# Optimization experiments

Measured on AMD Instinct MI355X. Metric: run time of the kernel, lower is better.

The kernel has to match this reference:

```python
import jax, jax.numpy as jnp
import numpy as np

B, D, K, L, C = 1024, 512, 255, 256, 80  # batch, feat, internal nodes, leaves, classes
DEPTH = 8  # complete binary tree: 2^8 = 256 leaves


def _build_res_path():
    # res_path[l, k] = 1 if internal node k is on leaf l's path and leaf goes left,
    # -1 if it goes right, 0 if node k not on the path (matches build_tree_squeeze).
    rp = np.zeros((L, K), dtype=np.int32)
    for leaf in range(L):
        node = 0
        for d in range(DEPTH):
            bit = (leaf >> (DEPTH - 1 - d)) & 1  # 0 -> left, 1 -> right
            rp[leaf, node] = 1 if bit == 0 else -1
            node = 2 * node + 1 + bit
    return jnp.asarray(rp)


def setup_inputs() -> dict:
    key = jax.random.key(0)
    k1, k2, k3, k4 = jax.random.split(key, 4)
    x = jax.random.normal(k1, (B, D), dtype=jnp.float32)
    node_embeddings = jax.random.normal(k2, (K, D), dtype=jnp.float32)
    leaf_W = jax.random.normal(k3, (L * C, D), dtype=jnp.float32) * (1.0 / np.sqrt(D))
    leaf_b = jax.random.normal(k4, (L * C,), dtype=jnp.float32) * 0.01
    res_path = _build_res_path()
    return {"x": x, "node_embeddings": node_embeddings, "leaf_W": leaf_W,
            "leaf_b": leaf_b, "res_path": res_path}


def reference(x, node_embeddings, leaf_W, leaf_b, res_path):
    # L2-normalize node embeddings, cosine-sim routing probabilities
    ne = node_embeddings / jnp.linalg.norm(node_embeddings, axis=-1, keepdims=True)
    node_sim = jax.nn.sigmoid(jnp.einsum('bc,kc->bk', x, ne))  # [B, K]
    # leaf decision logits: Linear(D, L*C) reshaped to [B, L, C]
    leaf_dec = (jnp.einsum('bc,oc->bo', x, leaf_W) + leaf_b).reshape(x.shape[0], L, C)
    left_mask = (res_path == 1)[None]    # [1, L, K]
    right_mask = (res_path == -1)[None]  # [1, L, K]
    ns = node_sim[:, None, :]            # [B, 1, K]
    prob_left = jnp.prod(jnp.where(left_mask, ns, 1.0), axis=-1)        # [B, L]
    prob_right = jnp.prod(jnp.where(right_mask, 1.0 - ns, 1.0), axis=-1)  # [B, L]
    probs = (prob_left * prob_right)[..., None] * leaf_dec  # [B, L, C]
    return probs.sum(axis=1), node_sim
```

## Files before the change

### kernel.cpp

```cpp
#include <hip/hip_runtime.h>
#include <stdint.h>

#define B_  1024
#define D_  512
#define K_  255
#define L_  256
#define C_  80

typedef __attribute__((ext_vector_type(8))) short bf16x8;
typedef __attribute__((ext_vector_type(4))) float f32x4;
typedef __attribute__((ext_vector_type(8))) short short8;

#define GLD(gsrc, ldst) \
  __builtin_amdgcn_global_load_lds((const __attribute__((address_space(1))) void*)(gsrc), \
                                   (__attribute__((address_space(3))) void*)(ldst), 16, 0, 0)

__device__ __forceinline__ short cvt_bf16(float f) {
    unsigned u = __float_as_uint(f);
    u += 0x7FFFu + ((u >> 16) & 1u);
    return (short)(u >> 16);
}

__global__ __launch_bounds__(256) void convert_kernel(const float* __restrict__ w,
                                                      const float* __restrict__ x,
                                                      const float* __restrict__ ne,
                                                      short* __restrict__ wb,
                                                      short* __restrict__ xb,
                                                      short* __restrict__ neb) {
    __shared__ float red[256];
    const int tid = threadIdx.x;
    if (blockIdx.x < 2048) {
        size_t i0 = (size_t)blockIdx.x * 256 + tid;
        const size_t stride = 2048u * 256u;
        for (size_t v = i0; v < 1310720u; v += stride) {
            float4 a = ((const float4*)w)[v * 2];
            float4 b = ((const float4*)w)[v * 2 + 1];
            short8 o;
            o[0] = cvt_bf16(a.x); o[1] = cvt_bf16(a.y); o[2] = cvt_bf16(a.z); o[3] = cvt_bf16(a.w);
            o[4] = cvt_bf16(b.x); o[5] = cvt_bf16(b.y); o[6] = cvt_bf16(b.z); o[7] = cvt_bf16(b.w);
            ((short8*)wb)[v] = o;
        }
        for (size_t v = i0; v < 65536u; v += stride) {
            float4 a = ((const float4*)x)[v * 2];
            float4 b = ((const float4*)x)[v * 2 + 1];
            short8 o;
            o[0] = cvt_bf16(a.x); o[1] = cvt_bf16(a.y); o[2] = cvt_bf16(a.z); o[3] = cvt_bf16(a.w);
            o[4] = cvt_bf16(b.x); o[5] = cvt_bf16(b.y); o[6] = cvt_bf16(b.z); o[7] = cvt_bf16(b.w);
            ((short8*)xb)[v] = o;
        }
    } else {
        const int row = blockIdx.x - 2048;
        if (row == 255) {
            ((unsigned*)(neb + 255 * 512))[tid] = 0u;
            return;
        }
        const float2* nr = (const float2*)(ne + (size_t)row * 512);
        float2 a = nr[tid];
        red[tid] = a.x * a.x + a.y * a.y;
        __syncthreads();
        #pragma unroll
        for (int s = 128; s > 0; s >>= 1) {
            if (tid < s) red[tid] += red[tid + s];
            __syncthreads();
        }
        float inv = rsqrtf(red[0]);
        unsigned lo = (unsigned short)cvt_bf16(a.x * inv);
        unsigned hi = (unsigned short)cvt_bf16(a.y * inv);
        ((unsigned*)(neb + (size_t)row * 512))[tid] = lo | (hi << 16);
    }
}

__global__ __launch_bounds__(256) void simgemm_kernel(const short* __restrict__ xb,
                                                      const short* __restrict__ neb,
                                                      float* __restrict__ out1) {
    __shared__ __align__(16) short Ald[512 * 8];
    __shared__ __align__(16) short Bld[512 * 8];
    const int tid = threadIdx.x;
    const int lane = tid & 63, wave = tid >> 6;
    const int q = lane >> 4, r = lane & 15;
    const int mt = blockIdx.x >> 2;
    const int nt = blockIdx.x & 3;

    f32x4 acc[4];
    #pragma unroll
    for (int nf = 0; nf < 4; ++nf) acc[nf] = (f32x4){0.f, 0.f, 0.f, 0.f};

    const bf16x8* Av = (const bf16x8*)Ald;
    const bf16x8* Bv = (const bf16x8*)Bld;

    for (int kb = 0; kb < 8; ++kb) {
        __syncthreads();
        #pragma unroll
        for (int j = 0; j < 2; ++j) {
            int ph = j * 256 + tid, rr = ph >> 3, g = (ph & 7) ^ (rr & 7);
            GLD(xb + ((size_t)(mt * 64 + rr) * D_ + kb * 64 + g * 8), Ald + ph * 8);
        }
        #pragma unroll
        for (int j = 0; j < 2; ++j) {
            int ph = j * 256 + tid, cc = ph >> 3, g = (ph & 7) ^ (cc & 7);
            GLD(neb + ((size_t)(nt * 64 + cc) * D_ + kb * 64 + g * 8), Bld + ph * 8);
        }
        __syncthreads();
        #pragma unroll
        for (int ks = 0; ks < 2; ++ks) {
            const int g = ks * 4 + q;
            int rl = wave * 16 + r;
            bf16x8 af = Av[rl * 8 + (g ^ (rl & 7))];
            #pragma unroll
            for (int nf = 0; nf < 4; ++nf) {
                int cl = nf * 16 + r;
                bf16x8 bfr = Bv[cl * 8 + (g ^ (cl & 7))];
                acc[nf] = __builtin_amdgcn_mfma_f32_16x16x32_bf16(af, bfr, acc[nf], 0, 0, 0);
            }
        }
    }
    #pragma unroll
    for (int nf = 0; nf < 4; ++nf) {
        int gcol = nt * 64 + nf * 16 + r;
        if (gcol < K_) {
            #pragma unroll
            for (int i = 0; i < 4; ++i) {
                int grow = mt * 64 + wave * 16 + q * 4 + i;
                out1[(size_t)grow * K_ + gcol] = 1.f / (1.f + __expf(-acc[nf][i]));
            }
        }
    }
}

__global__ __launch_bounds__(256) void leafprob_kernel(const float* __restrict__ out1,
                                                       float* __restrict__ p_ws,
                                                       float* __restrict__ out0) {
    __shared__ float ss[K_];
    const int b = blockIdx.x, t = threadIdx.x;
    if (t < K_) ss[t] = out1[(size_t)b * K_ + t];
    if (t < C_) out0[(size_t)b * C_ + t] = 0.f;
    __syncthreads();
    float prob = 1.f;
    int node = 0;
    #pragma unroll
    for (int d = 0; d < 8; ++d) {
        int bit = (t >> (7 - d)) & 1;
        float s = ss[node];
        prob *= bit ? (1.f - s) : s;
        node = 2 * node + 1 + bit;
    }
    p_ws[(size_t)b * L_ + t] = prob;
}

__global__ __launch_bounds__(256, 2) void gemm_kernel(const short* __restrict__ xb,
                                                      const short* __restrict__ wb,
                                                      const float* __restrict__ p,
                                                      const float* __restrict__ lb,
                                                      float* __restrict__ partial) {
    __shared__ __align__(16) short Ald[2 * 1024 * 8];
    __shared__ __align__(16) short Bld[2 * 640 * 8];
    __shared__ float p_ld[128][4];

    const int tid = threadIdx.x;
    const int lane = tid & 63, wave = tid >> 6;
    const int q = lane >> 4, r = lane & 15;
    const int wrow = wave * 32;
    const int lc = blockIdx.x & 63;
    const int mt = blockIdx.x >> 6;

    if (tid < 128) {
        float4 pw = *(const float4*)(p + (size_t)(mt * 128 + tid) * L_ + lc * 4);
        p_ld[tid][0] = pw.x; p_ld[tid][1] = pw.y;
        p_ld[tid][2] = pw.z; p_ld[tid][3] = pw.w;
    }

    auto stageA = [&](int buf, int kc) {
        #pragma unroll
        for (int j = 0; j < 4; ++j) {
            int ph = j * 256 + tid;
            int rr = ph >> 3;
            int g  = (ph & 7) ^ (rr & 7);
            GLD(xb + ((size_t)(mt * 128 + rr)) * D_ + kc * 64 + g * 8,
                Ald + (buf * 1024 + ph) * 8);
        }
    };
    auto stageB = [&](int buf, int li, int kc) {
        #pragma unroll
        for (int j = 0; j < 2; ++j) {
            int ph = j * 256 + tid;
            int cc = ph >> 3;
            int g  = (ph & 7) ^ (cc & 7);
            GLD(wb + ((size_t)(lc * 4 + li) * C_ + cc) * D_ + kc * 64 + g * 8,
                Bld + (buf * 640 + ph) * 8);
        }
        if (tid < 128) {
            int ph = 512 + tid;
            int cc = ph >> 3;
            int g  = (ph & 7) ^ (cc & 7);
            GLD(wb + ((size_t)(lc * 4 + li) * C_ + cc) * D_ + kc * 64 + g * 8,
                Bld + (buf * 640 + ph) * 8);
        }
    };

    stageA(0, 0);
    stageB(0, 0, 0);
    __syncthreads();

    f32x4 outacc[2][5];
    #pragma unroll
    for (int nf = 0; nf < 5; ++nf) {
        float bv[4];
        #pragma unroll
        for (int li = 0; li < 4; ++li)
            bv[li] = lb[(size_t)(lc * 4 + li) * C_ + nf * 16 + r];
        #pragma unroll
        for (int mf = 0; mf < 2; ++mf)
            #pragma unroll
            for (int i = 0; i < 4; ++i) {
                int row = wrow + mf * 16 + q * 4 + i;
                outacc[mf][nf][i] = p_ld[row][0] * bv[0] + p_ld[row][1] * bv[1]
                                  + p_ld[row][2] * bv[2] + p_ld[row][3] * bv[3];
            }
    }

    const f32x4 z4 = {0.f, 0.f, 0.f, 0.f};

    int abuf = 0, bbuf = 0;
    for (int kc = 0; kc < 8; ++kc) {
        #pragma unroll
        for (int li = 0; li < 4; ++li) {
            if (li < 3) {
                stageB(bbuf ^ 1, li + 1, kc);
            } else if (kc < 7) {
                stageB(bbuf ^ 1, 0, kc + 1);
                stageA(abuf ^ 1, kc + 1);
            }

            const bf16x8* Av = (const bf16x8*)Ald + abuf * 1024;
            const bf16x8* Bv = (const bf16x8*)Bld + bbuf * 640;

            f32x4 dec[2][5];
            #pragma unroll
            for (int ks = 0; ks < 2; ++ks) {
                const int g = ks * 4 + q;
                bf16x8 af[2], bfr[5];
                #pragma unroll
                for (int mf = 0; mf < 2; ++mf) {
                    int rl = wrow + mf * 16 + r;
                    af[mf] = Av[rl * 8 + (g ^ (rl & 7))];
                }
                #pragma unroll
                for (int nf = 0; nf < 5; ++nf) {
                    int cl = nf * 16 + r;
                    bfr[nf] = Bv[cl * 8 + (g ^ (cl & 7))];
                }
                #pragma unroll
                for (int mf = 0; mf < 2; ++mf)
                    #pragma unroll
                    for (int nf = 0; nf < 5; ++nf)
                        dec[mf][nf] = __builtin_amdgcn_mfma_f32_16x16x32_bf16(
                            af[mf], bfr[nf], ks == 0 ? z4 : dec[mf][nf], 0, 0, 0);
            }

            #pragma unroll
            for (int mf = 0; mf < 2; ++mf)
                #pragma unroll
                for (int i = 0; i < 4; ++i) {
                    float pf = p_ld[wrow + mf * 16 + q * 4 + i][li];
                    #pragma unroll
                    for (int nf = 0; nf < 5; ++nf)
                        outacc[mf][nf][i] += pf * dec[mf][nf][i];
                }

            __syncthreads();
            bbuf ^= 1;
            if (li == 3) abuf ^= 1;
        }
    }

    const size_t rbase = (size_t)lc * B_ + mt * 128;
    #pragma unroll
    for (int mf = 0; mf < 2; ++mf)
        #pragma unroll
        for (int nf = 0; nf < 5; ++nf)
            #pragma unroll
            for (int i = 0; i < 4; ++i) {
                int row = wrow + mf * 16 + q * 4 + i;
                int col = nf * 16 + r;
                partial[(rbase + row) * C_ + col] = outacc[mf][nf][i];
            }
}

__global__ __launch_bounds__(256) void reduce_kernel(const float* __restrict__ partial,
                                                     float* __restrict__ out0) {
    const int chunk = blockIdx.x >> 3;
    const int jg    = blockIdx.x & 7;
    const int idx   = chunk * 256 + threadIdx.x;
    const float4* p4 = (const float4*)partial;
    float4 s = {0.f, 0.f, 0.f, 0.f};
    #pragma unroll
    for (int j = 0; j < 8; ++j) {
        float4 v = p4[(size_t)(jg * 8 + j) * (B_ * C_ / 4) + idx];
        s.x += v.x; s.y += v.y; s.z += v.z; s.w += v.w;
    }
    float* o = out0 + (size_t)idx * 4;
    atomicAdd(o + 0, s.x);
    atomicAdd(o + 1, s.y);
    atomicAdd(o + 2, s.z);
    atomicAdd(o + 3, s.w);
}

extern "C" void kernel_launch(void* const* d_in, const int* in_sizes, int n_in,
                              void* d_out, int out_size, void* d_ws, size_t ws_size,
                              hipStream_t stream) {
    const float* x  = (const float*)d_in[0];
    const float* ne = (const float*)d_in[1];
    const float* lW = (const float*)d_in[2];
    const float* lb = (const float*)d_in[3];

    float* out0 = (float*)d_out;
    float* out1 = out0 + (size_t)B_ * C_;

    char* ws = (char*)d_ws;
    short* xb      = (short*)ws;
    short* neb     = (short*)(ws + (1u << 20));
    float* p_ws    = (float*)(ws + (1u << 20) + (1u << 18));
    short* wb      = (short*)(ws + (9u << 18));
    float* partial = (float*)(ws + (24u << 20));

    convert_kernel<<<2304, 256, 0, stream>>>(lW, x, ne, wb, xb, neb);
    simgemm_kernel<<<64, 256, 0, stream>>>(xb, neb, out1);
    leafprob_kernel<<<B_, 256, 0, stream>>>(out1, p_ws, out0);
    gemm_kernel<<<512, 256, 0, stream>>>(xb, wb, p_ws, lb, partial);
    reduce_kernel<<<640, 256, 0, stream>>>(partial, out0);
}
```

Baseline: 155.4 us.

## Triple-buffer leaf-weight tiles with vmcnt waits and fuse reduction via atomics

The leaf GEMM now stages weight tiles into a three-slot LDS ring instead of a double buffer. It synchronises with explicit s_waitcnt vmcnt counts plus raw barriers in place of __syncthreads, so loads for the tile two steps ahead stay in flight during MFMA work. The separate reduce kernel and the partial-sum workspace are dropped, and each block atomically adds its accumulator straight into the output. The bias init is also computed from global loads before staging begins. This trades a kernel launch and a large partial-buffer round trip for 64-way atomic contention on the output, more LDS per block, and fragile hand-tuned wait counts.

```diff
diff --git a/kernel.cpp b/kernel.cpp
--- a/kernel.cpp
+++ b/kernel.cpp
@@ -14,6 +14,12 @@
 #define GLD(gsrc, ldst) \
   __builtin_amdgcn_global_load_lds((const __attribute__((address_space(1))) void*)(gsrc), \
                                    (__attribute__((address_space(3))) void*)(ldst), 16, 0, 0)
+
+#define WAITV_(n) asm volatile("s_waitcnt vmcnt(" #n ")" ::: "memory")
+#define WAITV(n)  WAITV_(n)
+#define BARR() do { __builtin_amdgcn_s_barrier(); \
+                    asm volatile("" ::: "memory"); \
+                    __builtin_amdgcn_sched_barrier(0); } while (0)
 
 __device__ __forceinline__ short cvt_bf16(float f) {
     unsigned u = __float_as_uint(f);
@@ -151,9 +157,9 @@
                                                       const short* __restrict__ wb,
                                                       const float* __restrict__ p,
                                                       const float* __restrict__ lb,
-                                                      float* __restrict__ partial) {
+                                                      float* __restrict__ out0) {
     __shared__ __align__(16) short Ald[2 * 1024 * 8];
-    __shared__ __align__(16) short Bld[2 * 640 * 8];
+    __shared__ __align__(16) short Bld[3 * 768 * 8];
     __shared__ float p_ld[128][4];
 
     const int tid = threadIdx.x;
@@ -163,6 +169,23 @@
     const int lc = blockIdx.x & 63;
     const int mt = blockIdx.x >> 6;
 
+    f32x4 outacc[2][5];
+    #pragma unroll
+    for (int mf = 0; mf < 2; ++mf)
+        #pragma unroll
+        for (int i = 0; i < 4; ++i) {
+            int row = mt * 128 + wrow + mf * 16 + q * 4 + i;
+            float4 pw = *(const float4*)(p + (size_t)row * L_ + lc * 4);
+            #pragma unroll
+            for (int nf = 0; nf < 5; ++nf) {
+                float s = pw.x * lb[(size_t)(lc * 4 + 0) * C_ + nf * 16 + r]
+                        + pw.y * lb[(size_t)(lc * 4 + 1) * C_ + nf * 16 + r]
+                        + pw.z * lb[(size_t)(lc * 4 + 2) * C_ + nf * 16 + r]
+                        + pw.w * lb[(size_t)(lc * 4 + 3) * C_ + nf * 16 + r];
+                outacc[mf][nf][i] = s;
+            }
+        }
+
     if (tid < 128) {
         float4 pw = *(const float4*)(p + (size_t)(mt * 128 + tid) * L_ + lc * 4);
         p_ld[tid][0] = pw.x; p_ld[tid][1] = pw.y;
@@ -179,130 +202,108 @@
                 Ald + (buf * 1024 + ph) * 8);
         }
     };
-    auto stageB = [&](int buf, int li, int kc) {
-        #pragma unroll
-        for (int j = 0; j < 2; ++j) {
+    auto stageB = [&](int buf, int l, int kc) {
+        #pragma unroll
+        for (int j = 0; j < 3; ++j) {
             int ph = j * 256 + tid;
             int cc = ph >> 3;
             int g  = (ph & 7) ^ (cc & 7);
-            GLD(wb + ((size_t)(lc * 4 + li) * C_ + cc) * D_ + kc * 64 + g * 8,
-                Bld + (buf * 640 + ph) * 8);
-        }
-        if (tid < 128) {
-            int ph = 512 + tid;
-            int cc = ph >> 3;
-            int g  = (ph & 7) ^ (cc & 7);
-            GLD(wb + ((size_t)(lc * 4 + li) * C_ + cc) * D_ + kc * 64 + g * 8,
-                Bld + (buf * 640 + ph) * 8);
+            GLD(wb + ((size_t)l * C_ + cc) * D_ + kc * 64 + g * 8,
+                Bld + (buf * 768 + ph) * 8);
         }
     };
 
-    stageA(0, 0);
-    stageB(0, 0, 0);
-    __syncthreads();
-
-    f32x4 outacc[2][5];
-    #pragma unroll
-    for (int nf = 0; nf < 5; ++nf) {
-        float bv[4];
-        #pragma unroll
-        for (int li = 0; li < 4; ++li)
-            bv[li] = lb[(size_t)(lc * 4 + li) * C_ + nf * 16 + r];
-        #pragma unroll
-        for (int mf = 0; mf < 2; ++mf)
-            #pragma unroll
-            for (int i = 0; i < 4; ++i) {
-                int row = wrow + mf * 16 + q * 4 + i;
-                outacc[mf][nf][i] = p_ld[row][0] * bv[0] + p_ld[row][1] * bv[1]
-                                  + p_ld[row][2] * bv[2] + p_ld[row][3] * bv[3];
-            }
-    }
-
     const f32x4 z4 = {0.f, 0.f, 0.f, 0.f};
 
-    int abuf = 0, bbuf = 0;
-    for (int kc = 0; kc < 8; ++kc) {
-        #pragma unroll
-        for (int li = 0; li < 4; ++li) {
-            if (li < 3) {
-                stageB(bbuf ^ 1, li + 1, kc);
-            } else if (kc < 7) {
-                stageB(bbuf ^ 1, 0, kc + 1);
-                stageA(abuf ^ 1, kc + 1);
-            }
-
-            const bf16x8* Av = (const bf16x8*)Ald + abuf * 1024;
-            const bf16x8* Bv = (const bf16x8*)Bld + bbuf * 640;
-
-            f32x4 dec[2][5];
-            #pragma unroll
-            for (int ks = 0; ks < 2; ++ks) {
-                const int g = ks * 4 + q;
-                bf16x8 af[2], bfr[5];
-                #pragma unroll
-                for (int mf = 0; mf < 2; ++mf) {
-                    int rl = wrow + mf * 16 + r;
-                    af[mf] = Av[rl * 8 + (g ^ (rl & 7))];
-                }
-                #pragma unroll
-                for (int nf = 0; nf < 5; ++nf) {
-                    int cl = nf * 16 + r;
-                    bfr[nf] = Bv[cl * 8 + (g ^ (cl & 7))];
-                }
-                #pragma unroll
-                for (int mf = 0; mf < 2; ++mf)
-                    #pragma unroll
-                    for (int nf = 0; nf < 5; ++nf)
-                        dec[mf][nf] = __builtin_amdgcn_mfma_f32_16x16x32_bf16(
-                            af[mf], bfr[nf], ks == 0 ? z4 : dec[mf][nf], 0, 0, 0);
-            }
-
+    auto computeR = [&](int ab, int bb, int li) {
+        const bf16x8* Av = (const bf16x8*)Ald + ab * 1024;
+        const bf16x8* Bv = (const bf16x8*)Bld + bb * 768;
+        f32x4 dec[2][5];
+        #pragma unroll
+        for (int ks = 0; ks < 2; ++ks) {
+            const int g = ks * 4 + q;
+            bf16x8 af[2], bfr[5];
+            #pragma unroll
+            for (int mf = 0; mf < 2; ++mf) {
+                int rl = wrow + mf * 16 + r;
+                af[mf] = Av[rl * 8 + (g ^ (rl & 7))];
+            }
+            #pragma unroll
+            for (int nf = 0; nf < 5; ++nf) {
+                int cl = nf * 16 + r;
+                bfr[nf] = Bv[cl * 8 + (g ^ (cl & 7))];
+            }
             #pragma unroll
             for (int mf = 0; mf < 2; ++mf)
                 #pragma unroll
-                for (int i = 0; i < 4; ++i) {
-                    float pf = p_ld[wrow + mf * 16 + q * 4 + i][li];
-                    #pragma unroll
-                    for (int nf = 0; nf < 5; ++nf)
-                        outacc[mf][nf][i] += pf * dec[mf][nf][i];
-                }
-
-            __syncthreads();
-            bbuf ^= 1;
-            if (li == 3) abuf ^= 1;
-        }
-    }
-
-    const size_t rbase = (size_t)lc * B_ + mt * 128;
+                for (int nf = 0; nf < 5; ++nf)
+                    dec[mf][nf] = __builtin_amdgcn_mfma_f32_16x16x32_bf16(
+                        af[mf], bfr[nf], ks == 0 ? z4 : dec[mf][nf], 0, 0, 0);
+        }
+        #pragma unroll
+        for (int mf = 0; mf < 2; ++mf)
+            #pragma unroll
+            for (int i = 0; i < 4; ++i) {
+                float pf = p_ld[wrow + mf * 16 + q * 4 + i][li];
+                #pragma unroll
+                for (int nf = 0; nf < 5; ++nf)
+                    outacc[mf][nf][i] += pf * dec[mf][nf][i];
+            }
+    };
+
+    stageA(0, 0);
+    stageB(0, lc * 4 + 0, 0);
+    stageB(1, lc * 4 + 1, 0);
+    asm volatile("s_waitcnt lgkmcnt(0)" ::: "memory");
+
+    int bb = 0;
+    #define NX(b)  ((b) + 1 == 3 ? 0 : (b) + 1)
+    #define NX2(b) ((b) + 2 >= 3 ? (b) - 1 : (b) + 2)
+
+    for (int kc = 0; kc < 7; ++kc) {
+        const int ab = kc & 1;
+        WAITV(3); BARR();
+        stageB(NX2(bb), lc * 4 + 2, kc);
+        computeR(ab, bb, 0); bb = NX(bb);
+        WAITV(3); BARR();
+        stageB(NX2(bb), lc * 4 + 3, kc);
+        computeR(ab, bb, 1); bb = NX(bb);
+        WAITV(3); BARR();
+        stageB(NX2(bb), lc * 4 + 0, kc + 1);
+        stageA(ab ^ 1, kc + 1);
+        computeR(ab, bb, 2); bb = NX(bb);
+        WAITV(7); BARR();
+        stageB(NX2(bb), lc * 4 + 1, kc + 1);
+        computeR(ab, bb, 3); bb = NX(bb);
+    }
+    {
+        WAITV(3); BARR();
+        stageB(NX2(bb), lc * 4 + 2, 7);
+        computeR(1, bb, 0); bb = NX(bb);
+
+        WAITV(3); BARR();
+        stageB(NX2(bb), lc * 4 + 3, 7);
+        computeR(1, bb, 1); bb = NX(bb);
+
+        WAITV(3); BARR();
+        computeR(1, bb, 2); bb = NX(bb);
+
+        WAITV(0); BARR();
+        computeR(1, bb, 3);
+    }
+    #undef NX
+    #undef NX2
+
     #pragma unroll
     for (int mf = 0; mf < 2; ++mf)
         #pragma unroll
         for (int nf = 0; nf < 5; ++nf)
             #pragma unroll
             for (int i = 0; i < 4; ++i) {
-                int row = wrow + mf * 16 + q * 4 + i;
+                int row = mt * 128 + wrow + mf * 16 + q * 4 + i;
                 int col = nf * 16 + r;
-                partial[(rbase + row) * C_ + col] = outacc[mf][nf][i];
-            }
-}
-
-__global__ __launch_bounds__(256) void reduce_kernel(const float* __restrict__ partial,
-                                                     float* __restrict__ out0) {
-    const int chunk = blockIdx.x >> 3;
-    const int jg    = blockIdx.x & 7;
-    const int idx   = chunk * 256 + threadIdx.x;
-    const float4* p4 = (const float4*)partial;
-    float4 s = {0.f, 0.f, 0.f, 0.f};
-    #pragma unroll
-    for (int j = 0; j < 8; ++j) {
-        float4 v = p4[(size_t)(jg * 8 + j) * (B_ * C_ / 4) + idx];
-        s.x += v.x; s.y += v.y; s.z += v.z; s.w += v.w;
-    }
-    float* o = out0 + (size_t)idx * 4;
-    atomicAdd(o + 0, s.x);
-    atomicAdd(o + 1, s.y);
-    atomicAdd(o + 2, s.z);
-    atomicAdd(o + 3, s.w);
+                atomicAdd(out0 + (size_t)row * C_ + col, outacc[mf][nf][i]);
+            }
 }
 
 extern "C" void kernel_launch(void* const* d_in, const int* in_sizes, int n_in,
@@ -317,15 +318,13 @@
     float* out1 = out0 + (size_t)B_ * C_;
 
     char* ws = (char*)d_ws;
-    short* xb      = (short*)ws;
-    short* neb     = (short*)(ws + (1u << 20));
-    float* p_ws    = (float*)(ws + (1u << 20) + (1u << 18));
-    short* wb      = (short*)(ws + (9u << 18));
-    float* partial = (float*)(ws + (24u << 20));
+    short* xb   = (short*)ws;
+    short* neb  = (short*)(ws + (1u << 20));
+    float* p_ws = (float*)(ws + (1u << 20) + (1u << 18));
+    short* wb   = (short*)(ws + (9u << 18));
 
     convert_kernel<<<2304, 256, 0, stream>>>(lW, x, ne, wb, xb, neb);
     simgemm_kernel<<<64, 256, 0, stream>>>(xb, neb, out1);
     leafprob_kernel<<<B_, 256, 0, stream>>>(out1, p_ws, out0);
-    gemm_kernel<<<512, 256, 0, stream>>>(xb, wb, p_ws, lb, partial);
-    reduce_kernel<<<640, 256, 0, stream>>>(partial, out0);
-}
+    gemm_kernel<<<512, 256, 0, stream>>>(xb, wb, p_ws, lb, out0);
+}
```

After: 174.7 us. 12.4% more time.
